# Performance work log

Hardware: AMD Instinct MI355X
Metric: run time of the kernel (lower is better)

Reference implementation:

```python
import jax, jax.numpy as jnp
import numpy as np

B, T, C = 8, 2048, 1024
HEAD = 64


def setup_inputs() -> dict:
    key = jax.random.key(0)
    kx, kk, kq, kv = jax.random.split(key, 4)
    scale = 1.0 / np.sqrt(C)
    x = jax.random.normal(kx, (B, T, C), dtype=jnp.float32)
    # nn.Linear(n_embd, head_size, bias=False) weight shape: (head_size, n_embd)
    Wk = jax.random.normal(kk, (HEAD, C), dtype=jnp.float32) * scale
    Wq = jax.random.normal(kq, (HEAD, C), dtype=jnp.float32) * scale
    Wv = jax.random.normal(kv, (HEAD, C), dtype=jnp.float32) * scale
    return {"x": x, "Wk": Wk, "Wq": Wq, "Wv": Wv}


def reference(x, Wk, Wq, Wv):
    Bb, Tt, Cc = x.shape
    k = jnp.einsum('btc,hc->bth', x, Wk)  # (B,T,head)
    q = jnp.einsum('btc,hc->bth', x, Wq)
    v = jnp.einsum('btc,hc->bth', x, Wv)
    scaling = Cc ** (-0.5)  # NOTE: scales by full embed dim C, per source
    wei = jnp.einsum('bth,bsh->bts', q, k) * scaling  # (B,T,T)
    causal = jnp.tril(jnp.ones((Tt, Tt), dtype=bool))
    wei = jnp.where(causal, wei, -jnp.inf)
    wei = jax.nn.softmax(wei, axis=-1)  # stable max-subtract softmax (= _safe_softmax)
    out = jnp.einsum('bts,bsh->bth', wei, v)  # (B,T,head)
    return out
```

## Files before the change

### kernel.cpp

```cpp
#include <hip/hip_runtime.h>
#include <math.h>

#define B_ 8
#define T_ 2048
#define C_ 1024
#define H_ 64
#define M_ (B_ * T_)

typedef short bf8 __attribute__((ext_vector_type(8)));
typedef float f32x4 __attribute__((ext_vector_type(4)));

__device__ __forceinline__ unsigned short f2b(float f) {
    unsigned u = __float_as_uint(f);
    u += 0x7fffu + ((u >> 16) & 1u);
    return (unsigned short)(u >> 16);
}
__device__ __forceinline__ float b2f(unsigned short u) {
    return __uint_as_float(((unsigned)u) << 16);
}
__device__ __forceinline__ unsigned pack2(float lo, float hi) {
    unsigned a = __float_as_uint(lo) + 0x8000u;
    unsigned b = __float_as_uint(hi) + 0x8000u;
    return __builtin_amdgcn_perm(b, a, 0x07060302u);
}

__global__ __launch_bounds__(256) void wconv_kernel(
    const float* __restrict__ Wk, const float* __restrict__ Wq,
    const float* __restrict__ Wv, unsigned short* __restrict__ wP)
{
    int gid = blockIdx.x * 256 + threadIdx.x;
    int l   = gid & 63;
    int kk  = (gid >> 6) & 31;
    int jg  = gid >> 11;
    int m15 = l & 15, q4 = l >> 4;
    int n   = 16 * jg + m15;
    int c0  = 32 * kk + 8 * q4;
    const float* src;
    float scl;
    if (n < 64)       { src = Wq + (size_t)n * C_ + c0;        scl = 0.03125f; }
    else if (n < 128) { src = Wk + (size_t)(n - 64) * C_ + c0; scl = 1.0f; }
    else              { src = Wv + (size_t)(n - 128) * C_ + c0; scl = 1.0f; }
    float4 a = *(const float4*)src;
    float4 b = *(const float4*)(src + 4);
    ushort4 o0 = make_ushort4(f2b(a.x * scl), f2b(a.y * scl), f2b(a.z * scl), f2b(a.w * scl));
    ushort4 o1 = make_ushort4(f2b(b.x * scl), f2b(b.y * scl), f2b(b.z * scl), f2b(b.w * scl));
    *(ushort4*)(wP + (size_t)gid * 8)     = o0;
    *(ushort4*)(wP + (size_t)gid * 8 + 4) = o1;
}

__global__ __launch_bounds__(256) void qkv_kernel(
    const float* __restrict__ x, const unsigned short* __restrict__ wP,
    unsigned short* __restrict__ qo, unsigned short* __restrict__ kP,
    unsigned short* __restrict__ vP)
{
    __shared__ unsigned short As[2][32 * 64];

    const int tid  = threadIdx.x;
    const int lane = tid & 63;
    const int w    = tid >> 6;
    const int m15  = lane & 15;
    const int q4   = lane >> 4;
    const int r0   = blockIdx.x * 32;

    const int arow = tid >> 3;
    const int aoct = tid & 7;
    const float* xp = x + (size_t)(r0 + arow) * C_ + aoct * 8;
    const int awo = arow * 64 + ((aoct ^ (arow & 7)) * 8);

    const unsigned short* wbase = wP + ((size_t)(3 * w) * 2048 + lane) * 8;

    f32x4 acc[2][3];
#pragma unroll
    for (int i = 0; i < 2; ++i)
#pragma unroll
        for (int j = 0; j < 3; ++j) acc[i][j] = f32x4{0.f, 0.f, 0.f, 0.f};

    float4 xa0 = *(const float4*)xp;
    float4 xa1 = *(const float4*)(xp + 4);
    bf8 wreg[3][2];
#pragma unroll
    for (int j = 0; j < 3; ++j)
#pragma unroll
        for (int kc = 0; kc < 2; ++kc)
            wreg[j][kc] = *(const bf8*)(wbase + ((size_t)j * 2048 + kc * 64) * 8);

    {
        uint4 u = {pack2(xa0.x, xa0.y), pack2(xa0.z, xa0.w),
                   pack2(xa1.x, xa1.y), pack2(xa1.z, xa1.w)};
        *(uint4*)&As[0][awo] = u;
    }

    const int swz = m15 & 7;
    for (int ck = 0; ck < 16; ++ck) {
        const int nxt = ck + 1;
        float4 xb0, xb1;
        bf8 wn[3][2];
        if (nxt < 16) {
            xb0 = *(const float4*)(xp + nxt * 64);
            xb1 = *(const float4*)(xp + nxt * 64 + 4);
#pragma unroll
            for (int j = 0; j < 3; ++j)
#pragma unroll
                for (int kc = 0; kc < 2; ++kc)
                    wn[j][kc] = *(const bf8*)(wbase + ((size_t)j * 2048 + (2 * nxt + kc) * 64) * 8);
        }
        __syncthreads();
        const int buf = ck & 1;
#pragma unroll
        for (int kc = 0; kc < 2; ++kc) {
            bf8 af[2];
#pragma unroll
            for (int i = 0; i < 2; ++i)
                af[i] = *(const bf8*)&As[buf][(16 * i + m15) * 64 + (((4 * kc + q4) ^ swz) * 8)];
#pragma unroll
            for (int i = 0; i < 2; ++i)
#pragma unroll
                for (int j = 0; j < 3; ++j)
                    acc[i][j] = __builtin_amdgcn_mfma_f32_16x16x32_bf16(
                        af[i], wreg[j][kc], acc[i][j], 0, 0, 0);
        }
        if (nxt < 16) {
            uint4 u = {pack2(xb0.x, xb0.y), pack2(xb0.z, xb0.w),
                       pack2(xb1.x, xb1.y), pack2(xb1.z, xb1.w)};
            *(uint4*)&As[nxt & 1][awo] = u;
#pragma unroll
            for (int j = 0; j < 3; ++j)
#pragma unroll
                for (int kc = 0; kc < 2; ++kc) wreg[j][kc] = wn[j][kc];
        }
    }

#pragma unroll
    for (int i = 0; i < 2; ++i) {
#pragma unroll
        for (int j = 0; j < 3; ++j) {
            const int base = 48 * w + 16 * j;
            if (base < 64) {
#pragma unroll
                for (int r = 0; r < 4; ++r) {
                    int t = r0 + 16 * i + 4 * q4 + r;
                    qo[(size_t)t * H_ + base + m15] = f2b(acc[i][j][r]);
                }
            } else if (base < 128) {
                const int D0 = base - 64;
                const int f  = D0 >> 5;
                const int c1 = (D0 >> 3) & 3;
                const int l2 = (c1 + (m15 >> 3)) * 16;
#pragma unroll
                for (int r = 0; r < 4; ++r) {
                    int t  = r0 + 16 * i + 4 * q4 + r;
                    int bb = t >> 11, tt = t & 2047;
                    kP[(size_t)bb * 131072 +
                       (size_t)((((tt >> 4) * 2 + f) * 64 + l2 + (tt & 15)) * 8 + (m15 & 7))]
                        = f2b(acc[i][j][r]);
                }
            } else {
                const int cg = (base - 128) >> 4;
#pragma unroll
                for (int r = 0; r < 4; ++r) {
                    int t  = r0 + 16 * i + 4 * q4 + r;
                    int bb = t >> 11, tt = t & 2047;
                    int lv = ((tt & 31) >> 3) * 16 + m15;
                    vP[(size_t)bb * 131072 +
                       (size_t)((((tt >> 5) * 4 + cg) * 64 + lv) * 8 + (tt & 7))]
                        = f2b(acc[i][j][r]);
                }
            }
        }
    }
}

__global__ __launch_bounds__(512) void attn_kernel(
    const unsigned short* __restrict__ qo, const unsigned short* __restrict__ kP,
    const unsigned short* __restrict__ vP, float* __restrict__ outp)
{
    __shared__ unsigned short Pl[8][2][16 * 64];
    __shared__ float Ml[2][4][2][16];
    __shared__ unsigned short Ob[2][3][2][16 * 64];

    const int tid  = threadIdx.x;
    const int lane = tid & 63;
    const int w    = tid >> 6;
    const int m15  = lane & 15;
    const int q4   = lane >> 4;
    const int b    = blockIdx.x;
    const int y    = blockIdx.y;
    const int gsel = w >> 2;
    const int s    = w & 3;
    const int g    = gsel ? (63 - y) : y;
    const int trow = 32 * g;
    const int last = g >> 1;

    const unsigned short* qb = qo + (size_t)b * T_ * H_;
    const unsigned short* kb = kP + (size_t)b * 131072;
    const unsigned short* vb = vP + (size_t)b * 131072;

    bf8 qf[2][2];
#pragma unroll
    for (int gq = 0; gq < 2; ++gq)
#pragma unroll
        for (int f = 0; f < 2; ++f)
            qf[gq][f] = *(const bf8*)(qb + (size_t)(trow + 16 * gq + m15) * H_ + 32 * f + 8 * q4);

    f32x4 o[2][4];
#pragma unroll
    for (int gq = 0; gq < 2; ++gq)
#pragma unroll
        for (int cg = 0; cg < 4; ++cg) o[gq][cg] = f32x4{0.f, 0.f, 0.f, 0.f};
    float lr[2] = {0.f, 0.f};

    bf8 kf[4][2];
    if (s <= last) {
#pragma unroll
        for (int t2 = 0; t2 < 4; ++t2)
#pragma unroll
            for (int f = 0; f < 2; ++f)
                kf[t2][f] = *(const bf8*)(kb + (size_t)(((4 * s + t2) * 2 + f) * 64 + lane) * 8);
    }

    const int swz = m15 & 7;
    for (int kt = s; kt <= last; kt += 4) {
        const bool more = (kt + 4 <= last);
        bf8 kn[4][2];
        if (more) {
#pragma unroll
            for (int t2 = 0; t2 < 4; ++t2)
#pragma unroll
                for (int f = 0; f < 2; ++f)
                    kn[t2][f] = *(const bf8*)(kb + (size_t)(((4 * (kt + 4) + t2) * 2 + f) * 64 + lane) * 8);
        }
        bf8 vf[2][4];
#pragma unroll
        for (int kc = 0; kc < 2; ++kc)
#pragma unroll
            for (int cg = 0; cg < 4; ++cg)
                vf[kc][cg] = *(const bf8*)(vb + (size_t)(((2 * kt + kc) * 4 + cg) * 64 + lane) * 8);

#pragma unroll
        for (int gq = 0; gq < 2; ++gq) {
            f32x4 sa[4];
#pragma unroll
            for (int t2 = 0; t2 < 4; ++t2) sa[t2] = f32x4{0.f, 0.f, 0.f, 0.f};
#pragma unroll
            for (int t2 = 0; t2 < 4; ++t2)
#pragma unroll
                for (int f = 0; f < 2; ++f)
                    sa[t2] = __builtin_amdgcn_mfma_f32_16x16x32_bf16(
                        kf[t2][f], qf[gq][f], sa[t2], 0, 0, 0);

            if (kt == last) {
#pragma unroll
                for (int t2 = 0; t2 < 4; ++t2)
#pragma unroll
                    for (int r = 0; r < 4; ++r)
                        if (64 * kt + 16 * t2 + 4 * q4 + r > trow + 16 * gq + m15)
                            sa[t2][r] = -INFINITY;
            }

            float p[4][4];
            float sum = 0.f;
#pragma unroll
            for (int t2 = 0; t2 < 4; ++t2)
#pragma unroll
                for (int r = 0; r < 4; ++r) {
                    p[t2][r] = __expf(sa[t2][r]);
                    sum += p[t2][r];
                }
            lr[gq] += sum;

#pragma unroll
            for (int t2 = 0; t2 < 4; ++t2) {
                uint2 pk = {pack2(p[t2][0], p[t2][1]), pack2(p[t2][2], p[t2][3])};
                int c = 2 * t2 + (q4 >> 1);
                *(uint2*)&Pl[w][gq][m15 * 64 + ((c ^ swz) * 8) + (q4 & 1) * 4] = pk;
            }
            bf8 pf[2];
#pragma unroll
            for (int kc = 0; kc < 2; ++kc)
                pf[kc] = *(const bf8*)&Pl[w][gq][m15 * 64 + (((4 * kc + q4) ^ swz) * 8)];

#pragma unroll
            for (int cg = 0; cg < 4; ++cg) {
                o[gq][cg] = __builtin_amdgcn_mfma_f32_16x16x32_bf16(
                    pf[0], vf[0][cg], o[gq][cg], 0, 0, 0);
                o[gq][cg] = __builtin_amdgcn_mfma_f32_16x16x32_bf16(
                    pf[1], vf[1][cg], o[gq][cg], 0, 0, 0);
            }
        }

        if (more) {
#pragma unroll
            for (int t2 = 0; t2 < 4; ++t2)
#pragma unroll
                for (int f = 0; f < 2; ++f) kf[t2][f] = kn[t2][f];
        }
    }

#pragma unroll
    for (int gq = 0; gq < 2; ++gq) {
        lr[gq] += __shfl_xor(lr[gq], 16);
        lr[gq] += __shfl_xor(lr[gq], 32);
    }
    if (q4 == 0) {
#pragma unroll
        for (int gq = 0; gq < 2; ++gq) Ml[gsel][s][gq][m15] = lr[gq];
    }
    if (s >= 1) {
#pragma unroll
        for (int gq = 0; gq < 2; ++gq)
#pragma unroll
            for (int cg = 0; cg < 4; ++cg)
#pragma unroll
                for (int r = 0; r < 4; ++r)
                    Ob[gsel][s - 1][gq][(4 * q4 + r) * 64 + 16 * cg + m15] = f2b(o[gq][cg][r]);
    }
    __syncthreads();
    if (s == 0) {
        float* op = outp + (size_t)(b * T_ + trow) * H_;
#pragma unroll
        for (int gq = 0; gq < 2; ++gq) {
#pragma unroll
            for (int r = 0; r < 4; ++r) {
                const int qq = 4 * q4 + r;
                float L = Ml[gsel][0][gq][qq] + Ml[gsel][1][gq][qq]
                        + Ml[gsel][2][gq][qq] + Ml[gsel][3][gq][qq];
                float inv = 1.0f / L;
#pragma unroll
                for (int cg = 0; cg < 4; ++cg) {
                    float a = o[gq][cg][r];
#pragma unroll
                    for (int i = 1; i < 4; ++i)
                        a += b2f(Ob[gsel][i - 1][gq][qq * 64 + 16 * cg + m15]);
                    op[(size_t)(16 * gq + qq) * H_ + 16 * cg + m15] = a * inv;
                }
            }
        }
    }
}

extern "C" void kernel_launch(void* const* d_in, const int* in_sizes, int n_in,
                              void* d_out, int out_size, void* d_ws, size_t ws_size,
                              hipStream_t stream) {
    const float* x  = (const float*)d_in[0];
    const float* Wk = (const float*)d_in[1];
    const float* Wq = (const float*)d_in[2];
    const float* Wv = (const float*)d_in[3];
    char* ws = (char*)d_ws;
    unsigned short* wP = (unsigned short*)ws;
    unsigned short* qo = (unsigned short*)(ws + 0x080000);
    unsigned short* kP = (unsigned short*)(ws + 0x280000);
    unsigned short* vP = (unsigned short*)(ws + 0x480000);

    wconv_kernel<<<96, 256, 0, stream>>>(Wk, Wq, Wv, wP);
    qkv_kernel<<<M_ / 32, 256, 0, stream>>>(x, wP, qo, kP, vP);
    attn_kernel<<<dim3(8, 32), 512, 0, stream>>>(qo, kP, vP, (float*)d_out);
}
```

Before: 125.5 us.

## Balance waves between heavy and light query tiles and pack partial-output exchange

Each block pairs a heavy causal query tile (63-y) with a light one (y). It used to give each tile a fixed 4 waves; now it picks how many of the 8 waves go to each tile so that the longest per-wave KV loop is as short as possible. The goal is to remove the load imbalance where the heavy tile's waves gate the block's finish time. The cross-wave reduction of partial outputs now writes and reads packed bf16 as 16-byte vectors in lane order, instead of scattered 2-byte stores. The reduction loop length now varies per tile, which adds runtime loops and changes the shared-memory layout.

```diff
diff --git a/kernel.cpp b/kernel.cpp
--- a/kernel.cpp
+++ b/kernel.cpp
@@ -23,6 +23,8 @@
     unsigned b = __float_as_uint(hi) + 0x8000u;
     return __builtin_amdgcn_perm(b, a, 0x07060302u);
 }
+__device__ __forceinline__ float b2f_lo(unsigned u) { return __uint_as_float(u << 16); }
+__device__ __forceinline__ float b2f_hi(unsigned u) { return __uint_as_float(u & 0xffff0000u); }
 
 __global__ __launch_bounds__(256) void wconv_kernel(
     const float* __restrict__ Wk, const float* __restrict__ Wq,
@@ -175,8 +177,8 @@
     const unsigned short* __restrict__ vP, float* __restrict__ outp)
 {
     __shared__ unsigned short Pl[8][2][16 * 64];
-    __shared__ float Ml[2][4][2][16];
-    __shared__ unsigned short Ob[2][3][2][16 * 64];
+    __shared__ float Ml[2][8][2][16];
+    __shared__ unsigned short Ob[6][2][2][512];
 
     const int tid  = threadIdx.x;
     const int lane = tid & 63;
@@ -185,11 +187,24 @@
     const int q4   = lane >> 4;
     const int b    = blockIdx.x;
     const int y    = blockIdx.y;
-    const int gsel = w >> 2;
-    const int s    = w & 3;
-    const int g    = gsel ? (63 - y) : y;
-    const int trow = 32 * g;
-    const int last = g >> 1;
+
+    const int gh = 63 - y, gl = y;
+    const int nh = (gh >> 1) + 1;
+    const int nl = (gl >> 1) + 1;
+    int w1 = 1, bestc = 1 << 30;
+    for (int c = 1; c <= 7; ++c) {
+        int ch = (nh + c - 1) / c;
+        int cl = (nl + (7 - c)) / (8 - c);
+        int mx = ch > cl ? ch : cl;
+        if (mx < bestc) { bestc = mx; w1 = c; }
+    }
+    const bool heavy = (w < w1);
+    const int g     = heavy ? gh : gl;
+    const int rank  = heavy ? w : (w - w1);
+    const int nw    = heavy ? w1 : (8 - w1);
+    const int gidx  = heavy ? 0 : 1;
+    const int trow  = 32 * g;
+    const int last  = g >> 1;
 
     const unsigned short* qb = qo + (size_t)b * T_ * H_;
     const unsigned short* kb = kP + (size_t)b * 131072;
@@ -210,24 +225,24 @@
     float lr[2] = {0.f, 0.f};
 
     bf8 kf[4][2];
-    if (s <= last) {
+    if (rank <= last) {
 #pragma unroll
         for (int t2 = 0; t2 < 4; ++t2)
 #pragma unroll
             for (int f = 0; f < 2; ++f)
-                kf[t2][f] = *(const bf8*)(kb + (size_t)(((4 * s + t2) * 2 + f) * 64 + lane) * 8);
+                kf[t2][f] = *(const bf8*)(kb + (size_t)(((4 * rank + t2) * 2 + f) * 64 + lane) * 8);
     }
 
     const int swz = m15 & 7;
-    for (int kt = s; kt <= last; kt += 4) {
-        const bool more = (kt + 4 <= last);
+    for (int kt = rank; kt <= last; kt += nw) {
+        const bool more = (kt + nw <= last);
         bf8 kn[4][2];
         if (more) {
 #pragma unroll
             for (int t2 = 0; t2 < 4; ++t2)
 #pragma unroll
                 for (int f = 0; f < 2; ++f)
-                    kn[t2][f] = *(const bf8*)(kb + (size_t)(((4 * (kt + 4) + t2) * 2 + f) * 64 + lane) * 8);
+                    kn[t2][f] = *(const bf8*)(kb + (size_t)(((4 * (kt + nw) + t2) * 2 + f) * 64 + lane) * 8);
         }
         bf8 vf[2][4];
 #pragma unroll
@@ -302,37 +317,53 @@
         lr[gq] += __shfl_xor(lr[gq], 32);
     }
     if (q4 == 0) {
-#pragma unroll
-        for (int gq = 0; gq < 2; ++gq) Ml[gsel][s][gq][m15] = lr[gq];
-    }
-    if (s >= 1) {
-#pragma unroll
-        for (int gq = 0; gq < 2; ++gq)
-#pragma unroll
-            for (int cg = 0; cg < 4; ++cg)
-#pragma unroll
-                for (int r = 0; r < 4; ++r)
-                    Ob[gsel][s - 1][gq][(4 * q4 + r) * 64 + 16 * cg + m15] = f2b(o[gq][cg][r]);
+        Ml[gidx][rank][0][m15] = lr[0];
+        Ml[gidx][rank][1][m15] = lr[1];
+    }
+    if (rank >= 1) {
+        const int slice = heavy ? (rank - 1) : (w1 - 1 + rank - 1);
+#pragma unroll
+        for (int gq = 0; gq < 2; ++gq) {
+#pragma unroll
+            for (int h = 0; h < 2; ++h) {
+                uint4 u;
+                u.x = pack2(o[gq][2 * h + 0][0], o[gq][2 * h + 0][1]);
+                u.y = pack2(o[gq][2 * h + 0][2], o[gq][2 * h + 0][3]);
+                u.z = pack2(o[gq][2 * h + 1][0], o[gq][2 * h + 1][1]);
+                u.w = pack2(o[gq][2 * h + 1][2], o[gq][2 * h + 1][3]);
+                ((uint4*)&Ob[slice][gq][h][0])[lane] = u;
+            }
+        }
     }
     __syncthreads();
-    if (s == 0) {
+    if (rank == 0) {
         float* op = outp + (size_t)(b * T_ + trow) * H_;
 #pragma unroll
         for (int gq = 0; gq < 2; ++gq) {
+            for (int rr = 1; rr < nw; ++rr) {
+                const int slice = heavy ? (rr - 1) : (w1 - 1 + rr - 1);
+#pragma unroll
+                for (int h = 0; h < 2; ++h) {
+                    uint4 a = ((const uint4*)&Ob[slice][gq][h][0])[lane];
+                    o[gq][2 * h + 0][0] += b2f_lo(a.x);
+                    o[gq][2 * h + 0][1] += b2f_hi(a.x);
+                    o[gq][2 * h + 0][2] += b2f_lo(a.y);
+                    o[gq][2 * h + 0][3] += b2f_hi(a.y);
+                    o[gq][2 * h + 1][0] += b2f_lo(a.z);
+                    o[gq][2 * h + 1][1] += b2f_hi(a.z);
+                    o[gq][2 * h + 1][2] += b2f_lo(a.w);
+                    o[gq][2 * h + 1][3] += b2f_hi(a.w);
+                }
+            }
 #pragma unroll
             for (int r = 0; r < 4; ++r) {
                 const int qq = 4 * q4 + r;
-                float L = Ml[gsel][0][gq][qq] + Ml[gsel][1][gq][qq]
-                        + Ml[gsel][2][gq][qq] + Ml[gsel][3][gq][qq];
+                float L = 0.f;
+                for (int rr = 0; rr < nw; ++rr) L += Ml[gidx][rr][gq][qq];
                 float inv = 1.0f / L;
 #pragma unroll
-                for (int cg = 0; cg < 4; ++cg) {
-                    float a = o[gq][cg][r];
-#pragma unroll
-                    for (int i = 1; i < 4; ++i)
-                        a += b2f(Ob[gsel][i - 1][gq][qq * 64 + 16 * cg + m15]);
-                    op[(size_t)(16 * gq + qq) * H_ + 16 * cg + m15] = a * inv;
-                }
+                for (int cg = 0; cg < 4; ++cg)
+                    op[(size_t)(16 * gq + qq) * H_ + 16 * cg + m15] = o[gq][cg][r] * inv;
             }
         }
     }
```

Result: slower. 128.1 us (+2.0%).
